# Optimization experiments

Hardware: AMD Instinct MI355X
Metric: run time of the kernel (lower is better)

## Reference

```python
import jax, jax.numpy as jnp
import numpy as np

D = 384        # model dim
H = 6          # heads
HD = 64        # head dim (inner_dim = H*HD = 384)
DEPTH = 12
P = 16         # patch size
G = 14         # grid side (224/16)
NP = G * G     # 196 patches
NC = 1000
B = 64
DFF = 4 * D
SCALE = HD ** -0.5
EPS = 1e-5


def _ln(x, w, b):
    m = x.mean(-1, keepdims=True)
    v = ((x - m) ** 2).mean(-1, keepdims=True)
    return (x - m) * jax.lax.rsqrt(v + EPS) * w + b


def setup_inputs() -> dict:
    key = jax.random.key(0)
    ks = jax.random.split(key, 16)
    s = 0.02
    inp = {
        "x": jax.random.normal(ks[0], (B, 3, 224, 224), jnp.float32),
        # patch embedding conv as matmul: weight [3*P*P, D]
        "W_patch": jax.random.normal(ks[1], (3 * P * P, D), jnp.float32) * s,
        "b_patch": jnp.zeros((D,), jnp.float32),
        "ln0_w": jnp.ones((D,), jnp.float32),
        "ln0_b": jnp.zeros((D,), jnp.float32),
        "pos_emb": jax.random.normal(ks[2], (1, NP + 1, D), jnp.float32) * s,
        "cls_token": jax.random.normal(ks[3], (1, D), jnp.float32),
        # per-block params stacked over depth
        "ln1_w": jnp.ones((DEPTH, D), jnp.float32),
        "ln1_b": jnp.zeros((DEPTH, D), jnp.float32),
        "Wq": jax.random.normal(ks[4], (DEPTH, D, H * HD), jnp.float32) * s,
        "Wkv": jax.random.normal(ks[5], (DEPTH, D, 2 * H * HD), jnp.float32) * s,
        "Wo": jax.random.normal(ks[6], (DEPTH, H * HD, D), jnp.float32) * s,
        "bo": jnp.zeros((DEPTH, D), jnp.float32),
        "ln2_w": jnp.ones((DEPTH, D), jnp.float32),
        "ln2_b": jnp.zeros((DEPTH, D), jnp.float32),
        "W1": jax.random.normal(ks[7], (DEPTH, D, DFF), jnp.float32) * s,
        "b1": jnp.zeros((DEPTH, DFF), jnp.float32),
        "W2": jax.random.normal(ks[8], (DEPTH, DFF, D), jnp.float32) * s,
        "b2": jnp.zeros((DEPTH, D), jnp.float32),
        "lnf_w": jnp.ones((D,), jnp.float32),
        "lnf_b": jnp.zeros((D,), jnp.float32),
        "Whead": jax.random.normal(ks[9], (D, NC), jnp.float32) * s,
        "bhead": jnp.zeros((NC,), jnp.float32),
    }
    return inp


def reference(x, W_patch, b_patch, ln0_w, ln0_b, pos_emb, cls_token,
              ln1_w, ln1_b, Wq, Wkv, Wo, bo, ln2_w, ln2_b,
              W1, b1, W2, b2, lnf_w, lnf_b, Whead, bhead):
    b = x.shape[0]
    # patch embed: Conv2d(3, D, P, stride=P) == extract patches + matmul
    patches = x.reshape(b, 3, G, P, G, P).transpose(0, 2, 4, 1, 3, 5).reshape(b, NP, 3 * P * P)
    h = patches @ W_patch + b_patch                     # [b, NP, D]
    h = _ln(h, ln0_w, ln0_b)
    cls = jnp.broadcast_to(cls_token[None], (b, 1, D))
    h = jnp.concatenate([cls, h], axis=1) + pos_emb     # [b, NP+1, D]
    n = NP + 1
    for d in range(DEPTH):
        # self-attention with pre-LN, residual
        a = _ln(h, ln1_w[d], ln1_b[d])
        q = (a @ Wq[d]).reshape(b, n, H, HD).transpose(0, 2, 1, 3)
        kv = a @ Wkv[d]
        k = kv[..., : H * HD].reshape(b, n, H, HD).transpose(0, 2, 1, 3)
        v = kv[..., H * HD:].reshape(b, n, H, HD).transpose(0, 2, 1, 3)
        sim = jnp.einsum('bhid,bhjd->bhij', q, k) * SCALE
        attn = jax.nn.softmax(sim, axis=-1)
        o = jnp.einsum('bhij,bhjd->bhid', attn, v)
        o = o.transpose(0, 2, 1, 3).reshape(b, n, H * HD)
        h = h + o @ Wo[d] + bo[d]
        # MLP with pre-LN, residual, exact GELU
        m = _ln(h, ln2_w[d], ln2_b[d])
        m = jax.nn.gelu(m @ W1[d] + b1[d], approximate=False)
        h = h + m @ W2[d] + b2[d]
    cls_out = h[:, 0, :]
    logits = _ln(cls_out, lnf_w, lnf_b) @ Whead + bhead
    return logits
```

## Files before the change

### kernel.cpp

```cpp
#include <hip/hip_runtime.h>


typedef unsigned short u16;
typedef __attribute__((ext_vector_type(8))) short short8;
typedef __attribute__((ext_vector_type(4))) float f32x4;
typedef __attribute__((ext_vector_type(4))) unsigned short u16x4;
typedef __attribute__((ext_vector_type(2))) unsigned short u16x2;

#define D_      384
#define NH      6
#define DEPTH_  12
#define NP_     196
#define NT_     197
#define B_      64
#define DFF_    1536
#define M_REAL  (B_*NT_)
#define M_PAD   12672
#define M_PATCH (B_*NP_)

__device__ __forceinline__ float bf2f(u16 u){
  unsigned int i = ((unsigned int)u) << 16;
  return __builtin_bit_cast(float, i);
}
__device__ __forceinline__ u16 f2bf(float f){
  unsigned int i = __builtin_bit_cast(unsigned int, f);
  i = (i + 0x7FFFu + ((i >> 16) & 1u)) >> 16;
  return (u16)i;
}
__device__ __forceinline__ float gelu_f(float x){
  float t = x * (1.595769122f + 0.0713548162726f * x * x);
  return x / (1.f + __expf(-t));
}

#define GLOAD_LDS16(g, l) __builtin_amdgcn_global_load_lds( \
    (const __attribute__((address_space(1))) void*)(g),      \
    (__attribute__((address_space(3))) void*)(l), 16, 0, 0)

#define MFMA_BF16(a, b, c) __builtin_amdgcn_mfma_f32_16x16x32_bf16((a), (b), (c), 0, 0, 0)

struct TJobs {
  const float* src[7];
  u16*         dst[7];
  int          N[7], K[7], Nsrc[7];
  long long    ss[7], ds[7];
  int          cnt[7];
};

__global__ __launch_bounds__(256) void transpose_all(TJobs J)
{
  __shared__ float tile[32][33];
  int local = blockIdx.x;
  int j = 0;
  while (local >= J.cnt[j]) { local -= J.cnt[j]; ++j; }
  int nbx = J.N[j] >> 5, nby = J.K[j] >> 5;
  int z   = local / (nbx * nby);
  int rem = local - z * nbx * nby;
  int by = rem / nbx, bx = rem - by * nbx;
  const float* src = J.src[j] + (long long)z * J.ss[j];
  u16* dst = J.dst[j] + (long long)z * J.ds[j];
  int K = J.K[j], Nsrc = J.Nsrc[j];
  int tx = threadIdx.x, ty = threadIdx.y;
  int n0 = bx * 32, k0 = by * 32;
#pragma unroll
  for (int i = 0; i < 4; ++i){
    float v = 0.f;
    if (n0 + tx < Nsrc) v = src[(size_t)(k0 + ty + i*8) * Nsrc + n0 + tx];
    tile[ty + i*8][tx] = v;
  }
  __syncthreads();
#pragma unroll
  for (int i = 0; i < 4; ++i)
    dst[(size_t)(n0 + ty + i*8) * K + k0 + tx] = f2bf(tile[tx][ty + i*8]);
}

__global__ __launch_bounds__(256) void patch_extract(const float* __restrict__ x,
                                                     u16* __restrict__ patches)
{
  int r = blockIdx.x;
  int b = r / NP_, p = r % NP_;
  int gy = p / 14, gx = p % 14;
  int t = threadIdx.x;
  int py = t >> 4, px = t & 15;
#pragma unroll
  for (int c = 0; c < 3; ++c){
    float v = x[(((size_t)b*3 + c)*224 + gy*16 + py)*224 + gx*16 + px];
    patches[(size_t)r*768 + c*256 + t] = f2bf(v);
  }
}

template<int MODE, int BM, int BN, int KS, int NW>
__global__ __launch_bounds__(NW*64) void gemm_k(const u16* __restrict__ A,
                                                const u16* __restrict__ Bt,
                                                const float* __restrict__ bias,
                                                u16* __restrict__ outb,
                                                float* __restrict__ outf,
                                                int N, int K, int nbx, size_t sstride)
{
  constexpr int WAVES_M = (NW == 8) ? 4 : 2;
  constexpr int WM = BM / WAVES_M;
  constexpr int WN = BN / 2;
  constexpr int MI = WM / 16;
  constexpr int NJ = WN / 16;
  constexpr int CA = BM / (16 * NW);
  constexpr int CB = BN / (16 * NW);
  constexpr int L  = CA + CB;
  __shared__ u16 lds[2*(BM+BN)*32];
  u16* As = lds;
  u16* Bs = lds + 2*BM*32;
  int tid = threadIdx.x;
  int w = tid >> 6, lane = tid & 63;

  int nwg = gridDim.x;
  int q = nwg >> 3, r = nwg & 7;
  int xcd = blockIdx.x & 7, slot = blockIdx.x >> 3;
  int wgid = (xcd < r ? xcd*(q+1) : r*(q+1) + (xcd - r)*q) + slot;
  int m0 = (wgid / nbx) * BM;
  int n0 = (wgid % nbx) * BN;
  int kz = (KS > 1) ? blockIdx.y : 0;
  int Kl = K / KS;
  int koff = kz * Kl;
  int wr = w >> 1, wc = w & 1;

  f32x4 acc[MI][NJ];
#pragma unroll
  for (int i = 0; i < MI; ++i)
#pragma unroll
    for (int j = 0; j < NJ; ++j) acc[i][j] = (f32x4){0.f,0.f,0.f,0.f};

  int srow = lane >> 2;
  int skc  = ((lane & 3) ^ (srow & 3)) * 8;
  const u16* Ag = A  + (size_t)(m0 + w*16 + srow) * K + koff + skc;
  const u16* Bg = Bt + (size_t)(n0 + w*16 + srow) * K + koff + skc;

  int fr  = lane & 15;
  int fsw = ((lane >> 4) ^ (lane & 3)) << 3;

  auto stage = [&](int bi, int kt){
    u16* Ad = As + bi*(BM*32) + (w*16)*32;
    u16* Bd = Bs + bi*(BN*32) + (w*16)*32;
#pragma unroll
    for (int c = 0; c < CA; ++c)
      GLOAD_LDS16(Ag + (size_t)(c*16*NW)*K + kt, Ad + c*16*NW*32);
#pragma unroll
    for (int c = 0; c < CB; ++c)
      GLOAD_LDS16(Bg + (size_t)(c*16*NW)*K + kt, Bd + c*16*NW*32);
  };
  auto compute = [&](int bi){
    const u16* Ab = As + bi*(BM*32);
    const u16* Bb = Bs + bi*(BN*32);
    short8 af[MI], bfr[NJ];
#pragma unroll
    for (int i = 0; i < MI; ++i)
      af[i]  = *(const short8*)&Ab[(wr*WM + i*16 + fr)*32 + fsw];
#pragma unroll
    for (int j = 0; j < NJ; ++j)
      bfr[j] = *(const short8*)&Bb[(wc*WN + j*16 + fr)*32 + fsw];
#pragma unroll
    for (int i = 0; i < MI; ++i)
#pragma unroll
      for (int j = 0; j < NJ; ++j)
        acc[i][j] = MFMA_BF16(af[i], bfr[j], acc[i][j]);
  };

#define WAIT_L()  do { \
    if constexpr (L == 2)      asm volatile("s_waitcnt vmcnt(2)" ::: "memory"); \
    else if constexpr (L == 3) asm volatile("s_waitcnt vmcnt(3)" ::: "memory"); \
    else                       asm volatile("s_waitcnt vmcnt(4)" ::: "memory"); \
  } while (0)

  int nk = Kl >> 5;
  stage(0, 0);
  for (int t = 0; t < nk; t += 2){
    stage(1, (t + 1) * 32);
    __builtin_amdgcn_sched_barrier(0);
    WAIT_L();
    __builtin_amdgcn_s_barrier();
    asm volatile("" ::: "memory");
    compute(0);
    __builtin_amdgcn_sched_barrier(0);
    __builtin_amdgcn_s_barrier();
    if (t + 2 < nk){
      stage(0, (t + 2) * 32);
      __builtin_amdgcn_sched_barrier(0);
      WAIT_L();
    } else {
      __builtin_amdgcn_sched_barrier(0);
      asm volatile("s_waitcnt vmcnt(0)" ::: "memory");
    }
    __builtin_amdgcn_s_barrier();
    asm volatile("" ::: "memory");
    compute(1);
    __builtin_amdgcn_sched_barrier(0);
    __builtin_amdgcn_s_barrier();
  }
#undef WAIT_L

  int cr = (lane >> 4) << 2;
  int cc = lane & 15;

  if constexpr (MODE == 3){
#pragma unroll
    for (int j = 0; j < NJ; ++j){
      int c = n0 + wc*WN + j*16 + cc;
      float bv = bias ? bias[c] : 0.f;
#pragma unroll
      for (int i = 0; i < MI; ++i){
        int rbase = m0 + wr*WM + i*16 + cr;
#pragma unroll
        for (int e = 0; e < 4; ++e){
          float v = acc[i][j][e] + bv;
          if (c < N) outf[(size_t)(rbase + e) * N + c] = v;
        }
      }
    }
  } else {
    constexpr int PITCH = WN + 8;
    u16* Cs = lds + w * (16 * PITCH);
    u16* outp = (MODE == 4) ? outb + (size_t)kz * sstride : outb;
    int lr0 = lane >> 3;
    int lc  = lane & 7;
#pragma unroll
    for (int i = 0; i < MI; ++i){
#pragma unroll
      for (int j = 0; j < NJ; ++j){
        int c = n0 + wc*WN + j*16 + cc;
        float bv = (bias && kz == 0) ? bias[c] : 0.f;
#pragma unroll
        for (int e = 0; e < 4; ++e){
          float v = acc[i][j][e] + bv;
          if (MODE == 2) v = gelu_f(v);
          Cs[(cr + e) * PITCH + j*16 + cc] = f2bf(v);
        }
      }
#pragma unroll
      for (int p = 0; p < 2; ++p){
        int lr = p*8 + lr0;
        short8 val = *(const short8*)&Cs[lr * PITCH + lc*8];
        size_t gm = (size_t)(m0 + wr*WM + i*16 + lr);
        *(short8*)&outp[gm * N + n0 + wc*WN + lc*8] = val;
      }
    }
  }
}

__global__ __launch_bounds__(256) void ln_rows(const float* __restrict__ in,
                                               const float* __restrict__ gw,
                                               const float* __restrict__ gb,
                                               u16* __restrict__ out, int rows,
                                               size_t rstride)
{
  int m = blockIdx.x * 4 + (threadIdx.x >> 6);
  int lane = threadIdx.x & 63;
  if (m >= rows) return;
  const float* r = in + (size_t)m * rstride;
  float4 v0 = *(const float4*)(r + lane*4);
  float2 v1 = *(const float2*)(r + 256 + lane*2);
  float sum = v0.x+v0.y+v0.z+v0.w+v1.x+v1.y;
  float sq  = v0.x*v0.x+v0.y*v0.y+v0.z*v0.z+v0.w*v0.w+v1.x*v1.x+v1.y*v1.y;
#pragma unroll
  for (int d = 1; d < 64; d <<= 1){ sum += __shfl_xor(sum, d); sq += __shfl_xor(sq, d); }
  float mean = sum * (1.f/D_);
  float rs = rsqrtf(sq*(1.f/D_) - mean*mean + 1e-5f);
  float4 w0 = *(const float4*)(gw + lane*4);
  float2 w1 = *(const float2*)(gw + 256 + lane*2);
  float4 b0 = *(const float4*)(gb + lane*4);
  float2 b1v= *(const float2*)(gb + 256 + lane*2);
  u16x4 o4 = { f2bf((v0.x-mean)*rs*w0.x + b0.x), f2bf((v0.y-mean)*rs*w0.y + b0.y),
               f2bf((v0.z-mean)*rs*w0.z + b0.z), f2bf((v0.w-mean)*rs*w0.w + b0.w) };
  u16x2 o2 = { f2bf((v1.x-mean)*rs*w1.x + b1v.x), f2bf((v1.y-mean)*rs*w1.y + b1v.y) };
  *(u16x4*)(out + (size_t)m*D_ + lane*4) = o4;
  *(u16x2*)(out + (size_t)m*D_ + 256 + lane*2) = o2;
}

__global__ __launch_bounds__(256) void ln_rows_add(const float* __restrict__ in,
                                                   const u16* __restrict__ s0,
                                                   const u16* __restrict__ s1,
                                                   const float* __restrict__ gw,
                                                   const float* __restrict__ gb,
                                                   u16* __restrict__ out,
                                                   float* __restrict__ hout,
                                                   int rows, size_t rstride)
{
  int m = blockIdx.x * 4 + (threadIdx.x >> 6);
  int lane = threadIdx.x & 63;
  if (m >= rows) return;
  const float* r = in + (size_t)m * rstride;
  const u16* p0 = s0 + (size_t)m * rstride;
  const u16* p1 = s1 + (size_t)m * rstride;
  float4 v0 = *(const float4*)(r + lane*4);
  float2 v1 = *(const float2*)(r + 256 + lane*2);
  u16x4 a0 = *(const u16x4*)(p0 + lane*4);
  u16x2 a1 = *(const u16x2*)(p0 + 256 + lane*2);
  u16x4 c0 = *(const u16x4*)(p1 + lane*4);
  u16x2 c1 = *(const u16x2*)(p1 + 256 + lane*2);
  float x0 = v0.x + bf2f(a0.x) + bf2f(c0.x);
  float x1 = v0.y + bf2f(a0.y) + bf2f(c0.y);
  float x2 = v0.z + bf2f(a0.z) + bf2f(c0.z);
  float x3 = v0.w + bf2f(a0.w) + bf2f(c0.w);
  float x4 = v1.x + bf2f(a1.x) + bf2f(c1.x);
  float x5 = v1.y + bf2f(a1.y) + bf2f(c1.y);
  float sum = x0+x1+x2+x3+x4+x5;
  float sq  = x0*x0+x1*x1+x2*x2+x3*x3+x4*x4+x5*x5;
#pragma unroll
  for (int d = 1; d < 64; d <<= 1){ sum += __shfl_xor(sum, d); sq += __shfl_xor(sq, d); }
  float mean = sum * (1.f/D_);
  float rs = rsqrtf(sq*(1.f/D_) - mean*mean + 1e-5f);
  float4 w0 = *(const float4*)(gw + lane*4);
  float2 w1 = *(const float2*)(gw + 256 + lane*2);
  float4 b0 = *(const float4*)(gb + lane*4);
  float2 b1v= *(const float2*)(gb + 256 + lane*2);
  u16x4 o4 = { f2bf((x0-mean)*rs*w0.x + b0.x), f2bf((x1-mean)*rs*w0.y + b0.y),
               f2bf((x2-mean)*rs*w0.z + b0.z), f2bf((x3-mean)*rs*w0.w + b0.w) };
  u16x2 o2 = { f2bf((x4-mean)*rs*w1.x + b1v.x), f2bf((x5-mean)*rs*w1.y + b1v.y) };
  *(u16x4*)(out + (size_t)m*D_ + lane*4) = o4;
  *(u16x2*)(out + (size_t)m*D_ + 256 + lane*2) = o2;
  if (hout){
    float* ho = hout + (size_t)m * rstride;
    float4 h0 = {x0,x1,x2,x3};
    float2 h1 = {x4,x5};
    *(float4*)(ho + lane*4) = h0;
    *(float2*)(ho + 256 + lane*2) = h1;
  }
}

__global__ __launch_bounds__(256) void assemble_h(const u16* __restrict__ pe,
                                                  const float* __restrict__ gw,
                                                  const float* __restrict__ gb,
                                                  const float* __restrict__ pos,
                                                  const float* __restrict__ cls,
                                                  float* __restrict__ h)
{
  int m = blockIdx.x * 4 + (threadIdx.x >> 6);
  int lane = threadIdx.x & 63;
  if (m >= M_PAD) return;
  float* ho = h + (size_t)m * D_;
  if (m >= M_REAL){
    float4 z = {0.f,0.f,0.f,0.f};
    *(float4*)(ho + lane*4) = z;
    float2 z2 = {0.f,0.f};
    *(float2*)(ho + 256 + lane*2) = z2;
    return;
  }
  int b = m / NT_, t = m % NT_;
  const float* pr = pos + (size_t)t * D_;
  float4 p0 = *(const float4*)(pr + lane*4);
  float2 p1 = *(const float2*)(pr + 256 + lane*2);
  if (t == 0){
    float4 c0 = *(const float4*)(cls + lane*4);
    float2 c1 = *(const float2*)(cls + 256 + lane*2);
    float4 r0 = {c0.x+p0.x, c0.y+p0.y, c0.z+p0.z, c0.w+p0.w};
    float2 r1 = {c1.x+p1.x, c1.y+p1.y};
    *(float4*)(ho + lane*4) = r0;
    *(float2*)(ho + 256 + lane*2) = r1;
  } else {
    const u16* per = pe + (size_t)(b*NP_ + (t-1)) * D_;
    u16x4 a0 = *(const u16x4*)(per + lane*4);
    u16x2 a1 = *(const u16x2*)(per + 256 + lane*2);
    float x0=bf2f(a0.x), x1=bf2f(a0.y), x2=bf2f(a0.z), x3=bf2f(a0.w), x4=bf2f(a1.x), x5=bf2f(a1.y);
    float sum = x0+x1+x2+x3+x4+x5;
    float sq  = x0*x0+x1*x1+x2*x2+x3*x3+x4*x4+x5*x5;
#pragma unroll
    for (int d = 1; d < 64; d <<= 1){ sum += __shfl_xor(sum, d); sq += __shfl_xor(sq, d); }
    float mean = sum * (1.f/D_);
    float rs = rsqrtf(sq*(1.f/D_) - mean*mean + 1e-5f);
    float4 w0 = *(const float4*)(gw + lane*4);
    float2 w1 = *(const float2*)(gw + 256 + lane*2);
    float4 b0 = *(const float4*)(gb + lane*4);
    float2 b1v= *(const float2*)(gb + 256 + lane*2);
    float4 r0 = { (x0-mean)*rs*w0.x + b0.x + p0.x, (x1-mean)*rs*w0.y + b0.y + p0.y,
                  (x2-mean)*rs*w0.z + b0.z + p0.z, (x3-mean)*rs*w0.w + b0.w + p0.w };
    float2 r1 = { (x4-mean)*rs*w1.x + b1v.x + p1.x, (x5-mean)*rs*w1.y + b1v.y + p1.y };
    *(float4*)(ho + lane*4) = r0;
    *(float2*)(ho + 256 + lane*2) = r1;
  }
}

__global__ __launch_bounds__(256) void attn_k(const u16* __restrict__ qkv,
                                              u16* __restrict__ o)
{
  __shared__ u16 Ks[208*72];
  __shared__ u16 Vt[64*232];
  __shared__ u16 Ps[4][16*40];
  int bh = blockIdx.x;
  int b = bh / NH, hh = bh % NH;
  int tid = threadIdx.x, w = tid >> 6, lane = tid & 63;
  const u16* kbase = qkv + (size_t)b*NT_*1152 + 384 + hh*64;
  const u16* vbase = kbase + 384;

  int jr = tid >> 3, col = (tid & 7) * 8;
#pragma unroll
  for (int it = 0; it < 7; ++it){
    int j = it*32 + jr;
    if (j < 208){
      uint4 val = {0u,0u,0u,0u};
      if (j < 197) val = *(const uint4*)(kbase + (size_t)j*1152 + col);
      *(uint4*)&Ks[j*72 + col] = val;
    }
  }
#pragma unroll
  for (int it = 0; it < 7; ++it){
    int j = it*32 + jr;
    union { uint4 v; u16 s[8]; } u;
    u.v.x = 0u; u.v.y = 0u; u.v.z = 0u; u.v.w = 0u;
    if (j < 197) u.v = *(const uint4*)(vbase + (size_t)j*1152 + col);
#pragma unroll
    for (int e = 0; e < 8; ++e) Vt[(size_t)(col+e)*232 + j] = u.s[e];
  }
  __syncthreads();

  u16* myP = Ps[w];
  int fr = lane & 15, fk = lane >> 4;

  for (int qt = w; qt < 13; qt += 4){
    const u16* qrow = qkv + (size_t)(b*NT_ + qt*16 + fr)*1152 + hh*64 + fk*8;
    short8 aq0 = *(const short8*)qrow;
    short8 aq1 = *(const short8*)(qrow + 32);

    f32x4 s[13];
#pragma unroll
    for (int jt = 0; jt < 13; ++jt){
      const u16* kr = &Ks[(jt*16 + fr)*72 + fk*8];
      short8 bk0 = *(const short8*)kr;
      short8 bk1 = *(const short8*)(kr + 32);
      f32x4 z = {0.f,0.f,0.f,0.f};
      z = MFMA_BF16(aq0, bk0, z);
      z = MFMA_BF16(aq1, bk1, z);
      s[jt] = z;
    }

#pragma unroll
    for (int e = 0; e < 4; ++e){
      float mx = -1e30f;
#pragma unroll
      for (int jt = 0; jt < 13; ++jt){
        int cj = jt*16 + fr;
        float v = (cj < NT_) ? s[jt][e]*0.125f : -1e30f;
        s[jt][e] = v;
        mx = fmaxf(mx, v);
      }
#pragma unroll
      for (int d = 1; d < 16; d <<= 1) mx = fmaxf(mx, __shfl_xor(mx, d));
      float su = 0.f;
#pragma unroll
      for (int jt = 0; jt < 13; ++jt){
        float p = __expf(s[jt][e] - mx);
        s[jt][e] = p; su += p;
      }
#pragma unroll
      for (int d = 1; d < 16; d <<= 1) su += __shfl_xor(su, d);
      float ri = 1.f / su;
#pragma unroll
      for (int jt = 0; jt < 13; ++jt) s[jt][e] *= ri;
    }

    f32x4 oacc[4];
#pragma unroll
    for (int dt = 0; dt < 4; ++dt) oacc[dt] = (f32x4){0.f,0.f,0.f,0.f};
#pragma unroll
    for (int jc = 0; jc < 7; ++jc){
#pragma unroll
      for (int jtl = 0; jtl < 2; ++jtl){
        int jt = jc*2 + jtl;
#pragma unroll
        for (int e = 0; e < 4; ++e){
          u16 pv = 0;
          if (jt < 13) pv = f2bf(s[jt][e]);
          myP[(fk*4 + e)*40 + jtl*16 + fr] = pv;
        }
      }
      asm volatile("s_waitcnt lgkmcnt(0)" ::: "memory");
      short8 pa = *(const short8*)&myP[fr*40 + fk*8];
#pragma unroll
      for (int dt = 0; dt < 4; ++dt){
        short8 bv = *(const short8*)&Vt[(size_t)(dt*16 + fr)*232 + jc*32 + fk*8];
        oacc[dt] = MFMA_BF16(pa, bv, oacc[dt]);
      }
    }

#pragma unroll
    for (int dt = 0; dt < 4; ++dt)
#pragma unroll
      for (int e = 0; e < 4; ++e){
        int t = qt*16 + fk*4 + e;
        if (t < NT_)
          o[(size_t)(b*NT_ + t)*384 + hh*64 + dt*16 + fr] = f2bf(oacc[dt][e]);
      }
  }
}

extern "C" void kernel_launch(void* const* d_in, const int* in_sizes, int n_in,
                              void* d_out, int out_size, void* d_ws, size_t ws_size,
                              hipStream_t stream)
{
  (void)in_sizes; (void)n_in; (void)out_size; (void)ws_size;
  const float* x_in    = (const float*)d_in[0];
  const float* W_patch = (const float*)d_in[1];
  const float* b_patch = (const float*)d_in[2];
  const float* ln0_w   = (const float*)d_in[3];
  const float* ln0_b   = (const float*)d_in[4];
  const float* pos_emb = (const float*)d_in[5];
  const float* cls_tok = (const float*)d_in[6];
  const float* ln1_w   = (const float*)d_in[7];
  const float* ln1_b   = (const float*)d_in[8];
  const float* Wq      = (const float*)d_in[9];
  const float* Wkv     = (const float*)d_in[10];
  const float* Wo      = (const float*)d_in[11];
  const float* bo      = (const float*)d_in[12];
  const float* ln2_w   = (const float*)d_in[13];
  const float* ln2_b   = (const float*)d_in[14];
  const float* W1      = (const float*)d_in[15];
  const float* b1      = (const float*)d_in[16];
  const float* W2      = (const float*)d_in[17];
  const float* b2      = (const float*)d_in[18];
  const float* lnf_w   = (const float*)d_in[19];
  const float* lnf_b   = (const float*)d_in[20];
  const float* Whead   = (const float*)d_in[21];
  const float* bhead   = (const float*)d_in[22];

  char* ws = (char*)d_ws;
  size_t off = 0;
  auto nxt = [&](size_t bytes)->char* {
    char* p = ws + off;
    off += (bytes + 255) & ~(size_t)255;
    return p;
  };
  u16*   g_buf   = (u16*)  nxt((size_t)M_PAD * DFF_ * 2);
  float* hbuf    = (float*)nxt((size_t)M_PAD * D_ * 4);
  u16*   abuf    = (u16*)  nxt((size_t)M_PAD * D_ * 2);
  u16*   qkvbuf  = (u16*)  nxt((size_t)M_PAD * 1152 * 2);
  u16*   obuf    = (u16*)  nxt((size_t)M_PAD * D_ * 2);
  u16*   sbuf    = (u16*)  nxt((size_t)2 * M_PAD * D_ * 2);
  u16*   lncls   = (u16*)  nxt((size_t)B_ * D_ * 2);
  u16*   whT     = (u16*)  nxt((size_t)1024 * D_ * 2);
  u16*   wT      = (u16*)  nxt((size_t)21528576 * 2);

  const size_t SS = (size_t)M_PAD * D_;
  u16* patches = g_buf;
  u16* pebuf   = abuf;
  u16* wpT   = wT;
  u16* wqkvT = wpT   + 294912;
  u16* woT   = wqkvT + 12*442368;
  u16* w1T   = woT   + 12*147456;
  u16* w2T   = w1T   + 12*589824;

  TJobs J;
  auto setj = [&](int i, const float* s, u16* d, int N, int K, int Nsrc,
                  long long ss, long long ds, int nz){
    J.src[i]=s; J.dst[i]=d; J.N[i]=N; J.K[i]=K; J.Nsrc[i]=Nsrc;
    J.ss[i]=ss; J.ds[i]=ds; J.cnt[i]=(N/32)*(K/32)*nz;
  };
  setj(0, W_patch, wpT,             384,  768,  384, 0, 0, 1);
  setj(1, Wq,      wqkvT,           384,  384,  384, 384LL*384,  1152LL*384, 12);
  setj(2, Wkv,     wqkvT + 384*384, 768,  384,  768, 384LL*768,  1152LL*384, 12);
  setj(3, Wo,      woT,             384,  384,  384, 384LL*384,  384LL*384,  12);
  setj(4, W1,      w1T,             1536, 384, 1536, 384LL*1536, 384LL*1536, 12);
  setj(5, W2,      w2T,             384, 1536,  384, 1536LL*384, 1536LL*384, 12);
  setj(6, Whead,   whT,             1024, 384, 1000, 0, 0, 1);
  int tblocks = 0;
  for (int i = 0; i < 7; ++i) tblocks += J.cnt[i];
  transpose_all<<<tblocks, dim3(32,8), 0, stream>>>(J);

  patch_extract<<<M_PATCH, 256, 0, stream>>>(x_in, patches);
  gemm_k<0,128,128,1,8><<<3*(M_PATCH/128), 512, 0, stream>>>(patches, wpT, b_patch, pebuf, nullptr, 384, 768, 3, 0);
  assemble_h<<<M_PAD/4, 256, 0, stream>>>(pebuf, ln0_w, ln0_b, pos_emb, cls_tok, hbuf);

  for (int d = 0; d < DEPTH_; ++d){
    if (d == 0)
      ln_rows<<<M_PAD/4, 256, 0, stream>>>(hbuf, ln1_w, ln1_b, abuf, M_PAD, D_);
    else
      ln_rows_add<<<M_PAD/4, 256, 0, stream>>>(hbuf, sbuf, sbuf + SS,
                                               ln1_w + d*384, ln1_b + d*384,
                                               abuf, hbuf, M_PAD, D_);
    gemm_k<0,128,128,1,8><<<9*(M_PAD/128), 512, 0, stream>>>(abuf, wqkvT + (size_t)d*442368, nullptr, qkvbuf, nullptr, 1152, 384, 9, 0);
    attn_k<<<B_*NH, 256, 0, stream>>>(qkvbuf, obuf);
    gemm_k<4,128,128,2,8><<<dim3(3*(M_PAD/128), 2), 512, 0, stream>>>(obuf, woT + (size_t)d*147456, bo + d*384, sbuf, nullptr, 384, 384, 3, SS);
    ln_rows_add<<<M_PAD/4, 256, 0, stream>>>(hbuf, sbuf, sbuf + SS,
                                             ln2_w + d*384, ln2_b + d*384,
                                             abuf, hbuf, M_PAD, D_);
    gemm_k<2,128,128,1,8><<<12*(M_PAD/128), 512, 0, stream>>>(abuf, w1T + (size_t)d*589824, b1 + d*1536, g_buf, nullptr, 1536, 384, 12, 0);
    gemm_k<4,128,128,2,8><<<dim3(3*(M_PAD/128), 2), 512, 0, stream>>>(g_buf, w2T + (size_t)d*589824, b2 + d*384, sbuf, nullptr, 384, 1536, 3, SS);
  }

  ln_rows_add<<<B_/4, 256, 0, stream>>>(hbuf, sbuf, sbuf + SS,
                                        lnf_w, lnf_b, lncls, nullptr,
                                        B_, (size_t)NT_*D_);
  gemm_k<3,64,64,1,4><<<16, 256, 0, stream>>>(lncls, whT, bhead, nullptr, (float*)d_out, 1000, 384, 16, 0);
}
```

Baseline: 1.804 ms.

## Add 256x256 ping-pong MFMA GEMM for QKV and MLP-up projections

Introduces a new 256x256-tile, 8-wave GEMM kernel that double-buffers A/B in LDS with direct global-to-LDS loads, XOR-swizzled chunks, phased barriers with setprio, and an XCD-aware block remap. It replaces the 128x128 GEMM for the QKV and W1+GELU projections. QKV output is padded to 1280 columns so N divides 256, and M_PAD rises to 12800 to match 256-row tiles. The cost is extra padded work (wasted columns and rows) and a larger weight buffer, in exchange for more data reuse per tile and better load/compute overlap.

After: 2.000 ms. 1.11x slower.

```diff
diff --git a/kernel.cpp b/kernel.cpp
--- a/kernel.cpp
+++ b/kernel.cpp
@@ -14,8 +14,9 @@
 #define NT_     197
 #define B_      64
 #define DFF_    1536
+#define QS      1280
 #define M_REAL  (B_*NT_)
-#define M_PAD   12672
+#define M_PAD   12800
 #define M_PATCH (B_*NP_)
 
 __device__ __forceinline__ float bf2f(u16 u){
@@ -39,11 +40,11 @@
 #define MFMA_BF16(a, b, c) __builtin_amdgcn_mfma_f32_16x16x32_bf16((a), (b), (c), 0, 0, 0)
 
 struct TJobs {
-  const float* src[7];
-  u16*         dst[7];
-  int          N[7], K[7], Nsrc[7];
-  long long    ss[7], ds[7];
-  int          cnt[7];
+  const float* src[8];
+  u16*         dst[8];
+  int          N[8], K[8], Nsrc[8];
+  long long    ss[8], ds[8];
+  int          cnt[8];
 };
 
 __global__ __launch_bounds__(256) void transpose_all(TJobs J)
@@ -85,6 +86,223 @@
   for (int c = 0; c < 3; ++c){
     float v = x[(((size_t)b*3 + c)*224 + gy*16 + py)*224 + gx*16 + px];
     patches[(size_t)r*768 + c*256 + t] = f2bf(v);
+  }
+}
+
+template<int MODE>
+__global__ __launch_bounds__(512) void gemm8p(const u16* __restrict__ A,
+                                              const u16* __restrict__ Bt,
+                                              const float* __restrict__ bias,
+                                              u16* __restrict__ outb,
+                                              int N, int K, int nbx)
+{
+  __shared__ u16 lds[65536];
+  u16* Abuf[2] = { lds,         lds + 16384 };
+  u16* Bbuf[2] = { lds + 32768, lds + 49152 };
+  int tid = threadIdx.x, w = tid >> 6, lane = tid & 63;
+
+  int nwg = gridDim.x;
+  int q_ = nwg >> 3, r_ = nwg & 7;
+  int xcd = blockIdx.x & 7, slot = blockIdx.x >> 3;
+  int wgid = (xcd < r_ ? xcd*(q_+1) : r_*(q_+1) + (xcd - r_)*q_) + slot;
+  int m0 = (wgid / nbx) * 256;
+  int n0 = (wgid % nbx) * 256;
+  int wr = w >> 2, wc = w & 3;
+
+  f32x4 acc[8][4];
+#pragma unroll
+  for (int i = 0; i < 8; ++i)
+#pragma unroll
+    for (int j = 0; j < 4; ++j) acc[i][j] = (f32x4){0.f,0.f,0.f,0.f};
+
+  int l3 = lane >> 3, p8 = lane & 7;
+  int fr = lane & 15, fk = lane >> 4;
+  int frs = fr & 7;
+
+  auto stageA = [&](int buf, int half, int kt){
+    const u16* src = A + (size_t)(m0 + half*128) * K + kt;
+    u16* dst = Abuf[buf] + half*8192 + w*512;
+#pragma unroll
+    for (int g = 0; g < 2; ++g){
+      int row = g*64 + w*8 + l3;
+      int sc  = p8 ^ l3;
+      GLOAD_LDS16(src + (size_t)row*K + sc*8, dst + g*4096);
+    }
+  };
+  auto stageB = [&](int buf, int half, int kt){
+    const u16* src = Bt + (size_t)(n0 + half*128) * K + kt;
+    u16* dst = Bbuf[buf] + half*8192 + w*512;
+#pragma unroll
+    for (int g = 0; g < 2; ++g){
+      int row = g*64 + w*8 + l3;
+      int sc  = p8 ^ l3;
+      GLOAD_LDS16(src + (size_t)row*K + sc*8, dst + g*4096);
+    }
+  };
+  auto readA = [&](int buf, int qd, int h, short8* a4){
+#pragma unroll
+    for (int mi = 0; mi < 4; ++mi){
+      int ra = wr*128 + (qd*4 + mi)*16 + fr;
+      int ch = (h*4 + fk) ^ frs;
+      a4[mi] = *(const short8*)&Abuf[buf][ra*64 + ch*8];
+    }
+  };
+  auto readB = [&](int buf, short8 (*bf8)[2]){
+#pragma unroll
+    for (int nj = 0; nj < 4; ++nj)
+#pragma unroll
+      for (int h = 0; h < 2; ++h){
+        int rb = wc*64 + nj*16 + fr;
+        int ch = (h*4 + fk) ^ frs;
+        bf8[nj][h] = *(const short8*)&Bbuf[buf][rb*64 + ch*8];
+      }
+  };
+
+#define PH_OPEN() do { \
+    __builtin_amdgcn_sched_barrier(0); \
+    __builtin_amdgcn_s_barrier(); \
+    asm volatile("s_waitcnt lgkmcnt(0)" ::: "memory"); \
+    __builtin_amdgcn_sched_barrier(0); \
+    __builtin_amdgcn_s_setprio(1); \
+  } while (0)
+#define PH_CLOSE() do { \
+    __builtin_amdgcn_s_setprio(0); \
+    __builtin_amdgcn_sched_barrier(0); \
+    __builtin_amdgcn_s_barrier(); \
+    __builtin_amdgcn_sched_barrier(0); \
+  } while (0)
+#define PH_CLOSE_VM() do { \
+    __builtin_amdgcn_s_setprio(0); \
+    __builtin_amdgcn_sched_barrier(0); \
+    asm volatile("s_waitcnt vmcnt(4)" ::: "memory"); \
+    __builtin_amdgcn_s_barrier(); \
+    __builtin_amdgcn_sched_barrier(0); \
+  } while (0)
+
+  int nkt  = K >> 6;
+  int nfr  = nkt >> 1;
+
+  stageA(0, 0, 0); stageA(0, 1, 0);
+  stageB(0, 0, 0); stageB(0, 1, 0);
+  stageB(1, 0, 64); stageB(1, 1, 64);
+  __builtin_amdgcn_sched_barrier(0);
+  asm volatile("s_waitcnt vmcnt(4)" ::: "memory");
+  __builtin_amdgcn_s_barrier();
+  __builtin_amdgcn_sched_barrier(0);
+
+  short8 a4[4];
+  short8 bf8[4][2];
+
+  for (int f = 0; f < nfr; ++f){
+    int t   = 2*f;
+    int kt1 = (t+1)*64;
+    int kt2 = (t+2)*64; bool s2 = (t+2) < nkt;
+    int kt3 = (t+3)*64; bool s3 = (t+3) < nkt;
+
+    readA(0, 0, 0, a4); readB(0, bf8);
+    stageA(1, 0, kt1);
+    PH_OPEN();
+#pragma unroll
+    for (int mi = 0; mi < 4; ++mi)
+#pragma unroll
+      for (int nj = 0; nj < 4; ++nj)
+        acc[mi][nj] = MFMA_BF16(a4[mi], bf8[nj][0], acc[mi][nj]);
+    PH_CLOSE();
+    readA(0, 0, 1, a4);
+    stageA(1, 1, kt1);
+    PH_OPEN();
+#pragma unroll
+    for (int mi = 0; mi < 4; ++mi)
+#pragma unroll
+      for (int nj = 0; nj < 4; ++nj)
+        acc[mi][nj] = MFMA_BF16(a4[mi], bf8[nj][1], acc[mi][nj]);
+    PH_CLOSE();
+    readA(0, 1, 0, a4);
+    if (s2) stageB(0, 0, kt2);
+    PH_OPEN();
+#pragma unroll
+    for (int mi = 0; mi < 4; ++mi)
+#pragma unroll
+      for (int nj = 0; nj < 4; ++nj)
+        acc[4+mi][nj] = MFMA_BF16(a4[mi], bf8[nj][0], acc[4+mi][nj]);
+    PH_CLOSE();
+    readA(0, 1, 1, a4);
+    if (s2) stageB(0, 1, kt2);
+    PH_OPEN();
+#pragma unroll
+    for (int mi = 0; mi < 4; ++mi)
+#pragma unroll
+      for (int nj = 0; nj < 4; ++nj)
+        acc[4+mi][nj] = MFMA_BF16(a4[mi], bf8[nj][1], acc[4+mi][nj]);
+    PH_CLOSE_VM();
+
+    readA(1, 0, 0, a4); readB(1, bf8);
+    if (s2) stageA(0, 0, kt2);
+    PH_OPEN();
+#pragma unroll
+    for (int mi = 0; mi < 4; ++mi)
+#pragma unroll
+      for (int nj = 0; nj < 4; ++nj)
+        acc[mi][nj] = MFMA_BF16(a4[mi], bf8[nj][0], acc[mi][nj]);
+    PH_CLOSE();
+    readA(1, 0, 1, a4);
+    if (s2) stageA(0, 1, kt2);
+    PH_OPEN();
+#pragma unroll
+    for (int mi = 0; mi < 4; ++mi)
+#pragma unroll
+      for (int nj = 0; nj < 4; ++nj)
+        acc[mi][nj] = MFMA_BF16(a4[mi], bf8[nj][1], acc[mi][nj]);
+    PH_CLOSE();
+    readA(1, 1, 0, a4);
+    if (s3) stageB(1, 0, kt3);
+    PH_OPEN();
+#pragma unroll
+    for (int mi = 0; mi < 4; ++mi)
+#pragma unroll
+      for (int nj = 0; nj < 4; ++nj)
+        acc[4+mi][nj] = MFMA_BF16(a4[mi], bf8[nj][0], acc[4+mi][nj]);
+    PH_CLOSE();
+    readA(1, 1, 1, a4);
+    if (s3) stageB(1, 1, kt3);
+    PH_OPEN();
+#pragma unroll
+    for (int mi = 0; mi < 4; ++mi)
+#pragma unroll
+      for (int nj = 0; nj < 4; ++nj)
+        acc[4+mi][nj] = MFMA_BF16(a4[mi], bf8[nj][1], acc[4+mi][nj]);
+    PH_CLOSE_VM();
+  }
+#undef PH_OPEN
+#undef PH_CLOSE
+#undef PH_CLOSE_VM
+
+  __syncthreads();
+  int cr = (lane >> 4) << 2;
+  int cc = lane & 15;
+  constexpr int PITCH = 72;
+  u16* Cs = lds + w * (16 * PITCH);
+  int lr0 = lane >> 3, lc = lane & 7;
+#pragma unroll
+  for (int mi = 0; mi < 8; ++mi){
+#pragma unroll
+    for (int nj = 0; nj < 4; ++nj){
+      int c = n0 + wc*64 + nj*16 + cc;
+      float bv = bias ? bias[c] : 0.f;
+#pragma unroll
+      for (int e = 0; e < 4; ++e){
+        float v = acc[mi][nj][e] + bv;
+        if (MODE == 2) v = gelu_f(v);
+        Cs[(cr + e) * PITCH + nj*16 + cc] = f2bf(v);
+      }
+    }
+#pragma unroll
+    for (int p = 0; p < 2; ++p){
+      int lr = p*8 + lr0;
+      short8 val = *(const short8*)&Cs[lr * PITCH + lc*8];
+      size_t gm = (size_t)(m0 + wr*128 + mi*16 + lr);
+      *(short8*)&outb[gm * N + n0 + wc*64 + lc*8] = val;
+    }
   }
 }
 
@@ -384,7 +602,7 @@
   int bh = blockIdx.x;
   int b = bh / NH, hh = bh % NH;
   int tid = threadIdx.x, w = tid >> 6, lane = tid & 63;
-  const u16* kbase = qkv + (size_t)b*NT_*1152 + 384 + hh*64;
+  const u16* kbase = qkv + (size_t)b*NT_*QS + 384 + hh*64;
   const u16* vbase = kbase + 384;
 
   int jr = tid >> 3, col = (tid & 7) * 8;
@@ -393,7 +611,7 @@
     int j = it*32 + jr;
     if (j < 208){
       uint4 val = {0u,0u,0u,0u};
-      if (j < 197) val = *(const uint4*)(kbase + (size_t)j*1152 + col);
+      if (j < 197) val = *(const uint4*)(kbase + (size_t)j*QS + col);
       *(uint4*)&Ks[j*72 + col] = val;
     }
   }
@@ -402,7 +620,7 @@
     int j = it*32 + jr;
     union { uint4 v; u16 s[8]; } u;
     u.v.x = 0u; u.v.y = 0u; u.v.z = 0u; u.v.w = 0u;
-    if (j < 197) u.v = *(const uint4*)(vbase + (size_t)j*1152 + col);
+    if (j < 197) u.v = *(const uint4*)(vbase + (size_t)j*QS + col);
 #pragma unroll
     for (int e = 0; e < 8; ++e) Vt[(size_t)(col+e)*232 + j] = u.s[e];
   }
@@ -412,7 +630,7 @@
   int fr = lane & 15, fk = lane >> 4;
 
   for (int qt = w; qt < 13; qt += 4){
-    const u16* qrow = qkv + (size_t)(b*NT_ + qt*16 + fr)*1152 + hh*64 + fk*8;
+    const u16* qrow = qkv + (size_t)(b*NT_ + qt*16 + fr)*QS + hh*64 + fk*8;
     short8 aq0 = *(const short8*)qrow;
     short8 aq1 = *(const short8*)(qrow + 32);
 
@@ -527,19 +745,19 @@
   u16*   g_buf   = (u16*)  nxt((size_t)M_PAD * DFF_ * 2);
   float* hbuf    = (float*)nxt((size_t)M_PAD * D_ * 4);
   u16*   abuf    = (u16*)  nxt((size_t)M_PAD * D_ * 2);
-  u16*   qkvbuf  = (u16*)  nxt((size_t)M_PAD * 1152 * 2);
+  u16*   qkvbuf  = (u16*)  nxt((size_t)M_PAD * QS * 2);
   u16*   obuf    = (u16*)  nxt((size_t)M_PAD * D_ * 2);
   u16*   sbuf    = (u16*)  nxt((size_t)2 * M_PAD * D_ * 2);
   u16*   lncls   = (u16*)  nxt((size_t)B_ * D_ * 2);
   u16*   whT     = (u16*)  nxt((size_t)1024 * D_ * 2);
-  u16*   wT      = (u16*)  nxt((size_t)21528576 * 2);
+  u16*   wT      = (u16*)  nxt((size_t)22118400 * 2);
 
   const size_t SS = (size_t)M_PAD * D_;
   u16* patches = g_buf;
   u16* pebuf   = abuf;
   u16* wpT   = wT;
   u16* wqkvT = wpT   + 294912;
-  u16* woT   = wqkvT + 12*442368;
+  u16* woT   = wqkvT + 12*(QS*384);
   u16* w1T   = woT   + 12*147456;
   u16* w2T   = w1T   + 12*589824;
 
@@ -549,15 +767,16 @@
     J.src[i]=s; J.dst[i]=d; J.N[i]=N; J.K[i]=K; J.Nsrc[i]=Nsrc;
     J.ss[i]=ss; J.ds[i]=ds; J.cnt[i]=(N/32)*(K/32)*nz;
   };
-  setj(0, W_patch, wpT,             384,  768,  384, 0, 0, 1);
-  setj(1, Wq,      wqkvT,           384,  384,  384, 384LL*384,  1152LL*384, 12);
-  setj(2, Wkv,     wqkvT + 384*384, 768,  384,  768, 384LL*768,  1152LL*384, 12);
-  setj(3, Wo,      woT,             384,  384,  384, 384LL*384,  384LL*384,  12);
-  setj(4, W1,      w1T,             1536, 384, 1536, 384LL*1536, 384LL*1536, 12);
-  setj(5, W2,      w2T,             384, 1536,  384, 1536LL*384, 1536LL*384, 12);
-  setj(6, Whead,   whT,             1024, 384, 1000, 0, 0, 1);
+  setj(0, W_patch, wpT,               384,  768,  384, 0, 0, 1);
+  setj(1, Wq,      wqkvT,             384,  384,  384, 384LL*384,  (long long)QS*384, 12);
+  setj(2, Wkv,     wqkvT + 384*384,   768,  384,  768, 384LL*768,  (long long)QS*384, 12);
+  setj(3, Wq,      wqkvT + 1152*384,  128,  384,    0, 0,          (long long)QS*384, 12);
+  setj(4, Wo,      woT,               384,  384,  384, 384LL*384,  384LL*384,  12);
+  setj(5, W1,      w1T,               1536, 384, 1536, 384LL*1536, 384LL*1536, 12);
+  setj(6, W2,      w2T,               384, 1536,  384, 1536LL*384, 1536LL*384, 12);
+  setj(7, Whead,   whT,               1024, 384, 1000, 0, 0, 1);
   int tblocks = 0;
-  for (int i = 0; i < 7; ++i) tblocks += J.cnt[i];
+  for (int i = 0; i < 8; ++i) tblocks += J.cnt[i];
   transpose_all<<<tblocks, dim3(32,8), 0, stream>>>(J);
 
   patch_extract<<<M_PATCH, 256, 0, stream>>>(x_in, patches);
@@ -571,13 +790,13 @@
       ln_rows_add<<<M_PAD/4, 256, 0, stream>>>(hbuf, sbuf, sbuf + SS,
                                                ln1_w + d*384, ln1_b + d*384,
                                                abuf, hbuf, M_PAD, D_);
-    gemm_k<0,128,128,1,8><<<9*(M_PAD/128), 512, 0, stream>>>(abuf, wqkvT + (size_t)d*442368, nullptr, qkvbuf, nullptr, 1152, 384, 9, 0);
+    gemm8p<0><<<5*(M_PAD/256), 512, 0, stream>>>(abuf, wqkvT + (size_t)d*(QS*384), nullptr, qkvbuf, QS, 384, 5);
     attn_k<<<B_*NH, 256, 0, stream>>>(qkvbuf, obuf);
     gemm_k<4,128,128,2,8><<<dim3(3*(M_PAD/128), 2), 512, 0, stream>>>(obuf, woT + (size_t)d*147456, bo + d*384, sbuf, nullptr, 384, 384, 3, SS);
     ln_rows_add<<<M_PAD/4, 256, 0, stream>>>(hbuf, sbuf, sbuf + SS,
                                              ln2_w + d*384, ln2_b + d*384,
                                              abuf, hbuf, M_PAD, D_);
-    gemm_k<2,128,128,1,8><<<12*(M_PAD/128), 512, 0, stream>>>(abuf, w1T + (size_t)d*589824, b1 + d*1536, g_buf, nullptr, 1536, 384, 12, 0);
+    gemm8p<2><<<6*(M_PAD/256), 512, 0, stream>>>(abuf, w1T + (size_t)d*589824, b1 + d*1536, g_buf, 1536, 384, 6);
     gemm_k<4,128,128,2,8><<<dim3(3*(M_PAD/128), 2), 512, 0, stream>>>(g_buf, w2T + (size_t)d*589824, b2 + d*384, sbuf, nullptr, 384, 1536, 3, SS);
   }
 
```
